# Kernel tuning notes

Hardware: AMD Instinct MI355X
Metric: run time of the kernel (lower is better)

## Reference

```python
import jax, jax.numpy as jnp
import numpy as np

EPS = 1e-5
K = 5


def _bn(h, g, b):
    # BatchNorm1d in training mode: batch stats over all dims except channels.
    ax = tuple(range(h.ndim - 1))
    mu = jnp.mean(h, axis=ax, keepdims=True)
    var = jnp.var(h, axis=ax, keepdims=True)
    return g * (h - mu) * jax.lax.rsqrt(var + EPS) + b


def _block(x, w, b, g, be):
    # Lin -> ReLU -> BN, as in MLP() helper
    return _bn(jax.nn.relu(x @ w + b), g, be)


def _knn_idx(x, k):
    # x: [B, P, D]; k nearest per point (includes self at distance 0)
    sq = jnp.sum(x * x, axis=-1)
    d2 = sq[:, :, None] + sq[:, None, :] - 2.0 * jnp.einsum('bpd,bqd->bpq', x, x)
    return jax.lax.top_k(-d2, k)[1]  # [B, P, k]


def _edge_conv(x, k, mlp_fn):
    # DynamicEdgeConv: recompute kNN graph on current features, gather
    # neighbor/center pairs, per-edge MLP on [x_i, x_j - x_i], max-aggregate.
    idx = _knn_idx(x, k)                                   # [B,P,k]
    xj = jax.vmap(lambda xb, ib: xb[ib])(x, idx)           # [B,P,k,D]
    xi = jnp.broadcast_to(x[:, :, None, :], xj.shape)
    e = jnp.concatenate([xi, xj - xi], axis=-1)            # [B,P,k,2D]
    return jnp.max(mlp_fn(e), axis=2)                      # max aggr -> [B,P,C]


def dec_forward(pos,
                c1w0, c1b0, c1g0, c1e0,
                c1w1, c1b1, c1g1, c1e1,
                c1w2, c1b2, c1g2, c1e2,
                c2w, c2b, c2g, c2e,
                l1w, l1b, l1g, l1e,
                m1w, m1b, m1g, m1e,
                m2w, m2b, m2g, m2e,
                m3w, m3b):
    mlp1 = lambda e: _block(_block(_block(e, c1w0, c1b0, c1g0, c1e0),
                                   c1w1, c1b1, c1g1, c1e1),
                            c1w2, c1b2, c1g2, c1e2)
    x1 = _edge_conv(pos, K, mlp1)                          # [B,P,64]
    x2 = _edge_conv(x1, K, lambda e: _block(e, c2w, c2b, c2g, c2e))  # [B,P,128]
    h = _block(jnp.concatenate([x1, x2], axis=-1), l1w, l1b, l1g, l1e)  # [B,P,1024]
    p = jnp.max(h, axis=1)                                 # global_max_pool -> [B,1024]
    p = _block(p, m1w, m1b, m1g, m1e)                      # dropout omitted (eval)
    p = _block(p, m2w, m2b, m2g, m2e)
    return p @ m3w + m3b                                   # [B, n_classes]


def setup_inputs() -> dict:
    key = jax.random.key(0)
    ks = jax.random.split(key, 12)
    B, P = 16, 2048

    def w(k, shape):
        return 0.05 * jax.random.normal(k, shape, jnp.float32)

    z = lambda c: jnp.zeros((c,), jnp.float32)
    o = lambda c: jnp.ones((c,), jnp.float32)

    d = {
        'pos': jax.random.normal(ks[0], (B, P, 3), jnp.float32),
        'c1w0': w(ks[1], (6, 64)), 'c1b0': z(64), 'c1g0': o(64), 'c1e0': z(64),
        'c1w1': w(ks[2], (64, 64)), 'c1b1': z(64), 'c1g1': o(64), 'c1e1': z(64),
        'c1w2': w(ks[3], (64, 64)), 'c1b2': z(64), 'c1g2': o(64), 'c1e2': z(64),
        'c2w': w(ks[4], (128, 128)), 'c2b': z(128), 'c2g': o(128), 'c2e': z(128),
        'l1w': w(ks[5], (192, 1024)), 'l1b': z(1024), 'l1g': o(1024), 'l1e': z(1024),
        'm1w': w(ks[6], (1024, 512)), 'm1b': z(512), 'm1g': o(512), 'm1e': z(512),
        'm2w': w(ks[7], (512, 256)), 'm2b': z(256), 'm2g': o(256), 'm2e': z(256),
        'm3w': w(ks[8], (256, 2)), 'm3b': z(2),
    }
    return d


def reference(pos,
              c1w0, c1b0, c1g0, c1e0,
              c1w1, c1b1, c1g1, c1e1,
              c1w2, c1b2, c1g2, c1e2,
              c2w, c2b, c2g, c2e,
              l1w, l1b, l1g, l1e,
              m1w, m1b, m1g, m1e,
              m2w, m2b, m2g, m2e,
              m3w, m3b):
    return dec_forward(pos,
                       c1w0, c1b0, c1g0, c1e0,
                       c1w1, c1b1, c1g1, c1e1,
                       c1w2, c1b2, c1g2, c1e2,
                       c2w, c2b, c2g, c2e,
                       l1w, l1b, l1g, l1e,
                       m1w, m1b, m1g, m1e,
                       m2w, m2b, m2g, m2e,
                       m3w, m3b)
```

## Files before the change

### kernel.cpp

```cpp
#include <hip/hip_runtime.h>
#include <cmath>

constexpr int B = 16, P = 2048, KNN = 5;
constexpr int BP = B * P;
constexpr int E = BP * KNN;
constexpr float EPS = 1e-5f;
constexpr int AS = 72;
constexpr int QC2 = 4;

constexpr int ST0 = 0;
constexpr int ST1 = 128;
constexpr int ST2 = 256;
constexpr int ST3 = 384;
constexpr int ST4 = 640;
constexpr int ST5 = 2688;
constexpr int ST6 = 3712;
constexpr int ST_TOTAL = 4224;

typedef __attribute__((ext_vector_type(8))) short bf16x8;
typedef __attribute__((ext_vector_type(4))) float f32x4;

__device__ inline unsigned short f2bf(float x) {
    unsigned u = __float_as_uint(x);
    unsigned r = (u + 0x7FFFu + ((u >> 16) & 1u)) >> 16;
    return (unsigned short)r;
}
__device__ inline void split2bf(float x, unsigned short& h, unsigned short& l) {
    unsigned short hh = f2bf(x);
    float fh = __uint_as_float(((unsigned)hh) << 16);
    h = hh;
    l = f2bf(x - fh);
}
__device__ inline void packsplit(float a, float b, unsigned& hi2, unsigned& lo2) {
    unsigned short ah, al, bh, bl;
    split2bf(a, ah, al); split2bf(b, bh, bl);
    hi2 = (unsigned)ah | ((unsigned)bh << 16);
    lo2 = (unsigned)al | ((unsigned)bl << 16);
}

__device__ inline void ins5(float d, int qi, float bd[KNN], int bi[KNN]) {
    bool c0 = d < bd[0], c1 = d < bd[1], c2 = d < bd[2], c3 = d < bd[3], c4 = d < bd[4];
    bd[4] = c3 ? bd[3] : (c4 ? d : bd[4]);  bi[4] = c3 ? bi[3] : (c4 ? qi : bi[4]);
    bd[3] = c2 ? bd[2] : (c3 ? d : bd[3]);  bi[3] = c2 ? bi[2] : (c3 ? qi : bi[3]);
    bd[2] = c1 ? bd[1] : (c2 ? d : bd[2]);  bi[2] = c1 ? bi[1] : (c2 ? qi : bi[2]);
    bd[1] = c0 ? bd[0] : (c1 ? d : bd[1]);  bi[1] = c0 ? bi[0] : (c1 ? qi : bi[1]);
    bd[0] = c0 ? d : bd[0];                 bi[0] = c0 ? qi : bi[0];
}
__device__ inline void ins5t(float d, int qi, float bd[KNN], int bi[KNN]) {
    bool c0 = (d < bd[0]) || (d == bd[0] && qi < bi[0]);
    bool c1 = (d < bd[1]) || (d == bd[1] && qi < bi[1]);
    bool c2 = (d < bd[2]) || (d == bd[2] && qi < bi[2]);
    bool c3 = (d < bd[3]) || (d == bd[3] && qi < bi[3]);
    bool c4 = (d < bd[4]) || (d == bd[4] && qi < bi[4]);
    bd[4] = c3 ? bd[3] : (c4 ? d : bd[4]);  bi[4] = c3 ? bi[3] : (c4 ? qi : bi[4]);
    bd[3] = c2 ? bd[2] : (c3 ? d : bd[3]);  bi[3] = c2 ? bi[2] : (c3 ? qi : bi[3]);
    bd[2] = c1 ? bd[1] : (c2 ? d : bd[2]);  bi[2] = c1 ? bi[1] : (c2 ? qi : bi[2]);
    bd[1] = c0 ? bd[0] : (c1 ? d : bd[1]);  bi[1] = c0 ? bi[0] : (c1 ? qi : bi[1]);
    bd[0] = c0 ? d : bd[0];                 bi[0] = c0 ? qi : bi[0];
}

__global__ void k_init(float* __restrict__ stats, float* __restrict__ pmax,
                       float* __restrict__ pmin) {
    int i = blockIdx.x * 256 + threadIdx.x;
    if (i < ST_TOTAL) stats[i] = 0.f;
    if (i < B * 1024) { pmax[i] = 0.f; pmin[i] = INFINITY; }
}

__global__ __launch_bounds__(256) void k_redstat(const float* __restrict__ part,
        float* __restrict__ stats, int nblk) {
    __shared__ float r[256];
    int slot = blockIdx.x;
    float s = 0.f;
    for (int i = threadIdx.x; i < nblk; i += 256)
        s += part[(size_t)i * 128 + slot];
    r[threadIdx.x] = s; __syncthreads();
    for (int o = 128; o; o >>= 1) {
        if (threadIdx.x < o) r[threadIdx.x] += r[threadIdx.x + o];
        __syncthreads();
    }
    if (threadIdx.x == 0) stats[slot] = r[0];
}

__global__ void k_wsplit(const float* __restrict__ w, unsigned short* __restrict__ th,
                         unsigned short* __restrict__ tl, int K, int N) {
    int i = blockIdx.x * 256 + threadIdx.x;
    if (i >= K * N) return;
    int k = i / N, n = i - k * N;
    float f = w[i];
    unsigned short h = f2bf(f);
    th[(size_t)n * K + k] = h;
    tl[(size_t)n * K + k] = f2bf(f - __uint_as_float((unsigned)h << 16));
}

__global__ void k_xsplit(const float* __restrict__ x, unsigned short* __restrict__ xh,
                         unsigned short* __restrict__ xl) {
    int i = blockIdx.x * 256 + threadIdx.x;
    float f = x[i];
    unsigned short h = f2bf(f);
    xh[i] = h;
    xl[i] = f2bf(f - __uint_as_float((unsigned)h << 16));
}

__global__ __launch_bounds__(256) void k_knn1(const float* __restrict__ pos,
                                              int* __restrict__ idx1) {
    __shared__ float4 qt[2048];
    int b = blockIdx.x >> 5;
    int p0 = (blockIdx.x & 31) << 6;
    const float* posb = pos + (size_t)b * P * 3;
#pragma unroll
    for (int t = 0; t < 8; ++t) {
        int q = (t << 8) + threadIdx.x;
        float qx = posb[q * 3 + 0], qy = posb[q * 3 + 1], qz = posb[q * 3 + 2];
        qt[q] = make_float4(qx, qy, qz, qx * qx + qy * qy + qz * qz);
    }
    __syncthreads();
    int pl = threadIdx.x >> 2, sub = threadIdx.x & 3;
    int p = p0 + pl;
    float4 me = qt[p];
    float x = me.x, y = me.y, z = me.z, sqp = me.w;
    float bd[KNN]; int bi[KNN];
#pragma unroll
    for (int i = 0; i < KNN; ++i) { bd[i] = INFINITY; bi[i] = 0; }
    for (int j0 = 0; j0 < 512; j0 += 8) {
        float4 v[8];
#pragma unroll
        for (int u = 0; u < 8; ++u) v[u] = qt[((j0 + u) << 2) | sub];
#pragma unroll
        for (int u = 0; u < 8; ++u) {
            float dot = x * v[u].x + y * v[u].y + z * v[u].z;
            float d2 = sqp + v[u].w - 2.f * dot;
            if (d2 < bd[KNN - 1]) ins5(d2, ((j0 + u) << 2) | sub, bd, bi);
        }
    }
#pragma unroll
    for (int w = 1; w <= 2; w <<= 1) {
        float od[KNN]; int oi[KNN];
#pragma unroll
        for (int i = 0; i < KNN; ++i) {
            od[i] = __shfl_xor(bd[i], w, 64);
            oi[i] = __shfl_xor(bi[i], w, 64);
        }
#pragma unroll
        for (int i = 0; i < KNN; ++i) ins5t(od[i], oi[i], bd, bi);
    }
    if (sub == 0) {
        size_t o = ((size_t)b * P + p) * KNN;
#pragma unroll
        for (int i = 0; i < KNN; ++i) idx1[o + i] = bi[i];
    }
}

__global__ __launch_bounds__(256) void k_ec1_l0(const float* __restrict__ pos,
        const int* __restrict__ idx1, const float* __restrict__ w,
        const float* __restrict__ bias, float* __restrict__ zout,
        float* __restrict__ part) {
    __shared__ float elds[256][6];
    __shared__ float red[256];
    int tid = threadIdx.x;
    int base = blockIdx.x * 256;
    {
        int e = base + tid;
        int bp = e / KNN;
        int bb = bp >> 11;
        int q = idx1[e];
        const float* pi = pos + (size_t)bp * 3;
        const float* pj = pos + ((size_t)(bb << 11) + q) * 3;
        float x0 = pi[0], x1v = pi[1], x2v = pi[2];
        elds[tid][0] = x0; elds[tid][1] = x1v; elds[tid][2] = x2v;
        elds[tid][3] = pj[0] - x0; elds[tid][4] = pj[1] - x1v; elds[tid][5] = pj[2] - x2v;
    }
    int c = tid & 63, lane = tid >> 6;
    float wr[6];
#pragma unroll
    for (int d = 0; d < 6; ++d) wr[d] = w[d * 64 + c];
    float bc = bias[c];
    __syncthreads();
    float s1 = 0.f, s2 = 0.f;
    for (int i = 0; i < 64; ++i) {
        int e = lane + (i << 2);
        float acc = bc;
#pragma unroll
        for (int d = 0; d < 6; ++d) acc = fmaf(elds[e][d], wr[d], acc);
        acc = fmaxf(acc, 0.f);
        zout[(size_t)(base + e) * 64 + c] = acc;
        s1 += acc; s2 = fmaf(acc, acc, s2);
    }
    red[tid] = s1; __syncthreads();
    if (tid < 64) part[(size_t)blockIdx.x * 128 + tid] =
        red[tid] + red[tid + 64] + red[tid + 128] + red[tid + 192];
    __syncthreads();
    red[tid] = s2; __syncthreads();
    if (tid < 64) part[(size_t)blockIdx.x * 128 + 64 + tid] =
        red[tid] + red[tid + 64] + red[tid + 128] + red[tid + 192];
}

__global__ __launch_bounds__(256) void k_lin64(const float* __restrict__ zin,
        const float* __restrict__ statsIn, const float* __restrict__ g,
        const float* __restrict__ be, const float* __restrict__ w,
        const float* __restrict__ bias, float* __restrict__ zout,
        float* __restrict__ part, float invN) {
    __shared__ __align__(16) float a[64 * 64];
    __shared__ float scl[64], shf[64];
    __shared__ float red[256];
    int tid = threadIdx.x;
    int base = blockIdx.x * 64;
    if (tid < 64) {
        float mu = statsIn[tid] * invN;
        float var = statsIn[64 + tid] * invN - mu * mu;
        float sc = g[tid] * rsqrtf(var + EPS);
        scl[tid] = sc; shf[tid] = be[tid] - mu * sc;
    }
    __syncthreads();
#pragma unroll
    for (int t = 0; t < 16; ++t) {
        int flat = tid + (t << 8);
        int k = flat & 63;
        a[flat] = fmaf(zin[(size_t)base * 64 + flat], scl[k], shf[k]);
    }
    int c = tid & 63, lane = tid >> 6;
    float wr[64];
#pragma unroll
    for (int k = 0; k < 64; ++k) wr[k] = w[k * 64 + c];
    float bc = bias[c];
    __syncthreads();
    float s1 = 0.f, s2 = 0.f;
    for (int i = 0; i < 16; ++i) {
        int e = lane + (i << 2);
        const float4* ap4 = (const float4*)(a + (e << 6));
        float acc = bc;
#pragma unroll
        for (int k4 = 0; k4 < 16; ++k4) {
            float4 v = ap4[k4];
            acc = fmaf(v.x, wr[k4 * 4 + 0], acc);
            acc = fmaf(v.y, wr[k4 * 4 + 1], acc);
            acc = fmaf(v.z, wr[k4 * 4 + 2], acc);
            acc = fmaf(v.w, wr[k4 * 4 + 3], acc);
        }
        acc = fmaxf(acc, 0.f);
        zout[(size_t)(base + e) * 64 + c] = acc;
        s1 += acc; s2 = fmaf(acc, acc, s2);
    }
    red[tid] = s1; __syncthreads();
    if (tid < 64) part[(size_t)blockIdx.x * 128 + tid] =
        red[tid] + red[tid + 64] + red[tid + 128] + red[tid + 192];
    __syncthreads();
    red[tid] = s2; __syncthreads();
    if (tid < 64) part[(size_t)blockIdx.x * 128 + 64 + tid] =
        red[tid] + red[tid + 64] + red[tid + 128] + red[tid + 192];
}

__global__ __launch_bounds__(256) void k_ec1_fin(const float* __restrict__ z2,
        const float* __restrict__ statsIn, const float* __restrict__ g,
        const float* __restrict__ be, float* __restrict__ x1,
        float* __restrict__ sq2) {
    int tid = threadIdx.x;
    int o = blockIdx.x * 256 + tid;
    int c = o & 63; int bp = o >> 6;
    float mu = statsIn[c] * (1.f / E);
    float var = statsIn[64 + c] * (1.f / E) - mu * mu;
    float sc = g[c] * rsqrtf(var + EPS);
    float sh = be[c] - mu * sc;
    float m = -INFINITY;
#pragma unroll
    for (int j = 0; j < KNN; ++j)
        m = fmaxf(m, fmaf(z2[((size_t)bp * KNN + j) * 64 + c], sc, sh));
    x1[o] = m;
    float ss = m * m;
#pragma unroll
    for (int off = 32; off; off >>= 1) ss += __shfl_down(ss, off, 64);
    if (c == 0) sq2[bp] = ss;
}

__global__ __launch_bounds__(128, 1) void k_knn2(const unsigned short* __restrict__ x1h,
        const unsigned short* __restrict__ x1l, const float* __restrict__ sq2,
        float* __restrict__ cd, int* __restrict__ ci) {
    __shared__ float S[2][32 * 129];
    int tid = threadIdx.x;
    int wv = tid >> 6, lane = tid & 63;
    int l15 = lane & 15, quad = lane >> 4;
    int qc = blockIdx.x & (QC2 - 1);
    int pt = blockIdx.x >> 2;
    int b = pt >> 5;
    int pw = ((pt & 31) << 6) + wv * 32;
    const size_t xbase = (size_t)b * P * 64;
    float* Sw = &S[wv][0];

    bf16x8 ah[2][2], al[2][2];
#pragma unroll
    for (int i = 0; i < 2; ++i)
#pragma unroll
        for (int kc = 0; kc < 2; ++kc) {
            size_t o = xbase + (size_t)(pw + i * 16 + l15) * 64 + kc * 32 + quad * 8;
            ah[i][kc] = *(const bf16x8*)&x1h[o];
            al[i][kc] = *(const bf16x8*)&x1l[o];
        }

    int half = lane >> 5;
    int pidx = lane & 31;
    float bd[KNN]; int bi[KNN];
#pragma unroll
    for (int i = 0; i < KNN; ++i) { bd[i] = INFINITY; bi[i] = 0; }

    int qlo = qc << 9;
    for (int t = 0; t < 4; ++t) {
        int q0 = qlo + (t << 7);
        float qsv[8];
#pragma unroll
        for (int j = 0; j < 8; ++j) qsv[j] = sq2[b * P + q0 + j * 16 + l15];
        f32x4 acc[2][8];
#pragma unroll
        for (int i = 0; i < 2; ++i)
#pragma unroll
            for (int j = 0; j < 8; ++j) acc[i][j] = (f32x4)0.f;
#pragma unroll
        for (int kc = 0; kc < 2; ++kc) {
            bf16x8 bh[8], bl[8];
#pragma unroll
            for (int j = 0; j < 8; ++j) {
                size_t o = xbase + (size_t)(q0 + j * 16 + l15) * 64 + kc * 32 + quad * 8;
                bh[j] = *(const bf16x8*)&x1h[o];
                bl[j] = *(const bf16x8*)&x1l[o];
            }
#pragma unroll
            for (int i = 0; i < 2; ++i)
#pragma unroll
                for (int j = 0; j < 8; ++j) {
                    acc[i][j] = __builtin_amdgcn_mfma_f32_16x16x32_bf16(ah[i][kc], bh[j], acc[i][j], 0, 0, 0);
                    acc[i][j] = __builtin_amdgcn_mfma_f32_16x16x32_bf16(ah[i][kc], bl[j], acc[i][j], 0, 0, 0);
                    acc[i][j] = __builtin_amdgcn_mfma_f32_16x16x32_bf16(al[i][kc], bh[j], acc[i][j], 0, 0, 0);
                }
        }
#pragma unroll
        for (int i = 0; i < 2; ++i)
#pragma unroll
            for (int j = 0; j < 8; ++j)
#pragma unroll
                for (int r = 0; r < 4; ++r) {
                    int pl = i * 16 + quad * 4 + r;
                    Sw[pl * 129 + j * 16 + l15] = fmaf(acc[i][j][r], -2.f, qsv[j]);
                }
        const float* row = Sw + pidx * 129 + half * 64;
        int qb = q0 + half * 64;
        for (int jj = 0; jj < 64; jj += 4) {
            float k0 = row[jj + 0], k1 = row[jj + 1], k2 = row[jj + 2], k3 = row[jj + 3];
            if (k0 < bd[4]) ins5(k0, qb + jj + 0, bd, bi);
            if (k1 < bd[4]) ins5(k1, qb + jj + 1, bd, bi);
            if (k2 < bd[4]) ins5(k2, qb + jj + 2, bd, bi);
            if (k3 < bd[4]) ins5(k3, qb + jj + 3, bd, bi);
        }
    }
#pragma unroll
    for (int i = 0; i < KNN; ++i) {
        float od = __shfl_xor(bd[i], 32, 64);
        int oi = __shfl_xor(bi[i], 32, 64);
        if (half == 0) ins5t(od, oi, bd, bi);
    }
    if (half == 0) {
        size_t o = (((size_t)b * P + pw + pidx) * QC2 + qc) * KNN;
#pragma unroll
        for (int i = 0; i < KNN; ++i) { cd[o + i] = bd[i]; ci[o + i] = bi[i]; }
    }
}

__global__ __launch_bounds__(256) void k_knn2m(const float* __restrict__ cd,
        const int* __restrict__ ci, int* __restrict__ idx2) {
    int bp = blockIdx.x * 256 + threadIdx.x;
    float bd[KNN]; int bi[KNN];
#pragma unroll
    for (int i = 0; i < KNN; ++i) { bd[i] = INFINITY; bi[i] = 0; }
    size_t o = (size_t)bp * QC2 * KNN;
    for (int t = 0; t < QC2 * KNN; ++t) {
        float d2 = cd[o + t]; int qi = ci[o + t];
        if (d2 < bd[KNN - 1]) ins5(d2, qi, bd, bi);
    }
#pragma unroll
    for (int i = 0; i < KNN; ++i) idx2[bp * KNN + i] = bi[i];
}

__global__ __launch_bounds__(256) void k_ec2m(const float* __restrict__ x1,
        const int* __restrict__ idx2,
        const unsigned short* __restrict__ wth, const unsigned short* __restrict__ wtl,
        const float* __restrict__ bias, float* __restrict__ zout,
        float* __restrict__ stats) {
    __shared__ unsigned short Ah[128 * AS], Al[128 * AS];
    __shared__ int rowI[128], rowJ[128];
    __shared__ float red[2 * 128 * 2];
    int tid = threadIdx.x;
    int base = blockIdx.x * 128;
    int bb = base / (P * KNN);
    if (tid < 128) {
        int e = base + tid;
        int bp = e / KNN;
        rowI[tid] = bp;
        rowJ[tid] = (bb << 11) + idx2[e];
    }
    int wv = tid >> 6, lane = tid & 63;
    int wm = wv >> 1, wn = wv & 1;
    int l15 = lane & 15, quad = lane >> 4;
    f32x4 acc[4][4];
#pragma unroll
    for (int i = 0; i < 4; ++i)
#pragma unroll
        for (int j = 0; j < 4; ++j) acc[i][j] = (f32x4)0.f;

    for (int k0 = 0; k0 < 128; k0 += 64) {
        __syncthreads();
#pragma unroll
        for (int i = 0; i < 16; ++i) {
            int pr = tid + (i << 8);
            int r = pr >> 5, kp = (pr & 31) << 1;
            float2 vi = *(const float2*)(x1 + (size_t)rowI[r] * 64 + kp);
            float2 v;
            if (k0 == 0) v = vi;
            else {
                float2 vj = *(const float2*)(x1 + (size_t)rowJ[r] * 64 + kp);
                v = make_float2(vj.x - vi.x, vj.y - vi.y);
            }
            unsigned h2, l2; packsplit(v.x, v.y, h2, l2);
            *(unsigned*)&Ah[r * AS + kp] = h2;
            *(unsigned*)&Al[r * AS + kp] = l2;
        }
        __syncthreads();
#pragma unroll
        for (int kc = 0; kc < 64; kc += 32) {
            bf16x8 afh[4], afl[4], bfh[4], bfl[4];
#pragma unroll
            for (int i = 0; i < 4; ++i) {
                int ro = (wm * 64 + i * 16 + l15) * AS + kc + quad * 8;
                afh[i] = *(const bf16x8*)&Ah[ro];
                afl[i] = *(const bf16x8*)&Al[ro];
            }
#pragma unroll
            for (int j = 0; j < 4; ++j) {
                size_t wo = (size_t)(wn * 64 + j * 16 + l15) * 128 + k0 + kc + quad * 8;
                bfh[j] = *(const bf16x8*)&wth[wo];
                bfl[j] = *(const bf16x8*)&wtl[wo];
            }
#pragma unroll
            for (int i = 0; i < 4; ++i)
#pragma unroll
                for (int j = 0; j < 4; ++j) {
                    acc[i][j] = __builtin_amdgcn_mfma_f32_16x16x32_bf16(afh[i], bfh[j], acc[i][j], 0, 0, 0);
                    acc[i][j] = __builtin_amdgcn_mfma_f32_16x16x32_bf16(afh[i], bfl[j], acc[i][j], 0, 0, 0);
                    acc[i][j] = __builtin_amdgcn_mfma_f32_16x16x32_bf16(afl[i], bfh[j], acc[i][j], 0, 0, 0);
                }
        }
    }
#pragma unroll
    for (int j = 0; j < 4; ++j) {
        int colL = wn * 64 + j * 16 + l15;
        float bl = bias[colL];
        float s1 = 0.f, s2 = 0.f;
#pragma unroll
        for (int i = 0; i < 4; ++i) {
            int row = wm * 64 + i * 16 + quad * 4;
#pragma unroll
            for (int r = 0; r < 4; ++r) {
                float v = fmaxf(acc[i][j][r] + bl, 0.f);
                zout[(size_t)(base + row + r) * 128 + colL] = v;
                s1 += v; s2 = fmaf(v, v, s2);
            }
        }
        s1 += __shfl_xor(s1, 16, 64); s1 += __shfl_xor(s1, 32, 64);
        s2 += __shfl_xor(s2, 16, 64); s2 += __shfl_xor(s2, 32, 64);
        if (quad == 0) {
            red[(wm * 128 + colL) * 2 + 0] = s1;
            red[(wm * 128 + colL) * 2 + 1] = s2;
        }
    }
    __syncthreads();
    if (tid < 128) {
        atomicAdd(&stats[tid], red[tid * 2] + red[(128 + tid) * 2]);
        atomicAdd(&stats[128 + tid], red[tid * 2 + 1] + red[(128 + tid) * 2 + 1]);
    }
}

__global__ __launch_bounds__(256) void k_ec2_fin(const float* __restrict__ z3,
        const float* __restrict__ stats, const float* __restrict__ g,
        const float* __restrict__ be, float* __restrict__ x2) {
    int o = blockIdx.x * 256 + threadIdx.x;
    int c = o & 127; int bp = o >> 7;
    float mu = stats[c] * (1.f / E);
    float var = stats[128 + c] * (1.f / E) - mu * mu;
    float sc = g[c] * rsqrtf(var + EPS);
    float sh = be[c] - mu * sc;
    float m = -INFINITY;
#pragma unroll
    for (int j = 0; j < KNN; ++j)
        m = fmaxf(m, fmaf(z3[((size_t)bp * KNN + j) * 128 + c], sc, sh));
    x2[o] = m;
}

__global__ __launch_bounds__(256) void k_l1m(
        const unsigned short* __restrict__ x1h, const unsigned short* __restrict__ x1l,
        const unsigned short* __restrict__ x2h, const unsigned short* __restrict__ x2l,
        const unsigned short* __restrict__ wth, const unsigned short* __restrict__ wtl,
        const float* __restrict__ bias, float* __restrict__ stats,
        float* __restrict__ pmax, float* __restrict__ pmin) {
    __shared__ float red[2 * 128 * 4];
    int tid = threadIdx.x;
    int brow = blockIdx.x & 255;
    int bcol = blockIdx.x >> 8;
    int row0 = brow << 7, col0 = bcol << 7;
    int wv = tid >> 6, lane = tid & 63;
    int wm = wv >> 1, wn = wv & 1;
    int l15 = lane & 15, quad = lane >> 4;
    f32x4 acc[4][4];
#pragma unroll
    for (int i = 0; i < 4; ++i)
#pragma unroll
        for (int j = 0; j < 4; ++j) acc[i][j] = (f32x4)0.f;

#pragma unroll
    for (int k0 = 0; k0 < 192; k0 += 32) {
        const unsigned short* ah = (k0 < 64) ? x1h : x2h;
        const unsigned short* al = (k0 < 64) ? x1l : x2l;
        int astr = (k0 < 64) ? 64 : 128;
        int aoff = (k0 < 64) ? k0 : (k0 - 64);
        bf16x8 afh[4], afl[4], bfh[4], bfl[4];
#pragma unroll
        for (int i = 0; i < 4; ++i) {
            size_t o = (size_t)(row0 + wm * 64 + i * 16 + l15) * astr + aoff + quad * 8;
            afh[i] = *(const bf16x8*)&ah[o];
            afl[i] = *(const bf16x8*)&al[o];
        }
#pragma unroll
        for (int j = 0; j < 4; ++j) {
            size_t wo = (size_t)(col0 + wn * 64 + j * 16 + l15) * 192 + k0 + quad * 8;
            bfh[j] = *(const bf16x8*)&wth[wo];
            bfl[j] = *(const bf16x8*)&wtl[wo];
        }
#pragma unroll
        for (int i = 0; i < 4; ++i)
#pragma unroll
            for (int j = 0; j < 4; ++j) {
                acc[i][j] = __builtin_amdgcn_mfma_f32_16x16x32_bf16(afh[i], bfh[j], acc[i][j], 0, 0, 0);
                acc[i][j] = __builtin_amdgcn_mfma_f32_16x16x32_bf16(afh[i], bfl[j], acc[i][j], 0, 0, 0);
                acc[i][j] = __builtin_amdgcn_mfma_f32_16x16x32_bf16(afl[i], bfh[j], acc[i][j], 0, 0, 0);
            }
    }
#pragma unroll
    for (int j = 0; j < 4; ++j) {
        int colL = wn * 64 + j * 16 + l15;
        float bl = bias[col0 + colL];
        float s1 = 0.f, s2 = 0.f, mx = 0.f, mn = INFINITY;
#pragma unroll
        for (int i = 0; i < 4; ++i)
#pragma unroll
            for (int r = 0; r < 4; ++r) {
                float v = fmaxf(acc[i][j][r] + bl, 0.f);
                s1 += v; s2 = fmaf(v, v, s2);
                mx = fmaxf(mx, v); mn = fminf(mn, v);
            }
        s1 += __shfl_xor(s1, 16, 64); s1 += __shfl_xor(s1, 32, 64);
        s2 += __shfl_xor(s2, 16, 64); s2 += __shfl_xor(s2, 32, 64);
        mx = fmaxf(mx, __shfl_xor(mx, 16, 64)); mx = fmaxf(mx, __shfl_xor(mx, 32, 64));
        mn = fminf(mn, __shfl_xor(mn, 16, 64)); mn = fminf(mn, __shfl_xor(mn, 32, 64));
        if (quad == 0) {
            float* rp = &red[(wm * 128 + colL) * 4];
            rp[0] = s1; rp[1] = s2; rp[2] = mx; rp[3] = mn;
        }
    }
    __syncthreads();
    if (tid < 128) {
        const float* r0 = &red[tid * 4];
        const float* r1 = &red[(128 + tid) * 4];
        int bb = row0 >> 11;
        atomicAdd(&stats[col0 + tid], r0[0] + r1[0]);
        atomicAdd(&stats[1024 + col0 + tid], r0[1] + r1[1]);
        atomicMax((unsigned int*)&pmax[bb * 1024 + col0 + tid],
                  __float_as_uint(fmaxf(r0[2], r1[2])));
        atomicMin((unsigned int*)&pmin[bb * 1024 + col0 + tid],
                  __float_as_uint(fminf(r0[3], r1[3])));
    }
}

__global__ void k_pool(const float* __restrict__ stats, const float* __restrict__ g,
                       const float* __restrict__ be, const float* __restrict__ pmax,
                       const float* __restrict__ pmin, float* __restrict__ p) {
    int o = blockIdx.x * 256 + threadIdx.x;
    int c = o & 1023;
    float mu = stats[c] * (1.f / BP);
    float var = stats[1024 + c] * (1.f / BP) - mu * mu;
    float sc = g[c] * rsqrtf(var + EPS);
    float sh = be[c] - mu * sc;
    float v = (sc >= 0.f) ? pmax[o] : pmin[o];
    p[o] = fmaf(v, sc, sh);
}

__global__ __launch_bounds__(256) void k_m1(const float* __restrict__ p,
        const float* __restrict__ w, const float* __restrict__ bias,
        float* __restrict__ t1, float* __restrict__ stats) {
    int o = blockIdx.x * 256 + threadIdx.x;
    int c = o & 511, b = o >> 9;
    const float* pr = p + (b << 10);
    float acc = bias[c];
    for (int k = 0; k < 1024; ++k) acc = fmaf(pr[k], w[k * 512 + c], acc);
    acc = fmaxf(acc, 0.f);
    t1[o] = acc;
    atomicAdd(&stats[c], acc);
    atomicAdd(&stats[512 + c], acc * acc);
}

__global__ __launch_bounds__(256) void k_m2(const float* __restrict__ t1,
        const float* __restrict__ stats5, const float* __restrict__ g,
        const float* __restrict__ be, const float* __restrict__ w,
        const float* __restrict__ bias, float* __restrict__ t2,
        float* __restrict__ stats6) {
    __shared__ float scl[512], shf[512];
    int tid = threadIdx.x;
    for (int t = tid; t < 512; t += 256) {
        float mu = stats5[t] * (1.f / 16.f);
        float var = stats5[512 + t] * (1.f / 16.f) - mu * mu;
        float sc = g[t] * rsqrtf(var + EPS);
        scl[t] = sc; shf[t] = be[t] - mu * sc;
    }
    __syncthreads();
    int o = blockIdx.x * 256 + tid;
    int c = o & 255, b = o >> 8;
    const float* tr = t1 + (b << 9);
    float acc = bias[c];
    for (int k = 0; k < 512; ++k) {
        float u = fmaf(tr[k], scl[k], shf[k]);
        acc = fmaf(u, w[k * 256 + c], acc);
    }
    acc = fmaxf(acc, 0.f);
    t2[o] = acc;
    atomicAdd(&stats6[c], acc);
    atomicAdd(&stats6[256 + c], acc * acc);
}

__global__ __launch_bounds__(256) void k_m3(const float* __restrict__ t2,
        const float* __restrict__ stats6, const float* __restrict__ g,
        const float* __restrict__ be, const float* __restrict__ w,
        const float* __restrict__ bias, float* __restrict__ out) {
    __shared__ float scl[256], shf[256];
    int tid = threadIdx.x;
    {
        float mu = stats6[tid] * (1.f / 16.f);
        float var = stats6[256 + tid] * (1.f / 16.f) - mu * mu;
        float sc = g[tid] * rsqrtf(var + EPS);
        scl[tid] = sc; shf[tid] = be[tid] - mu * sc;
    }
    __syncthreads();
    if (tid < 32) {
        int c = tid & 1, b = tid >> 1;
        const float* tr = t2 + (b << 8);
        float acc = bias[c];
        for (int k = 0; k < 256; ++k) {
            float u = fmaf(tr[k], scl[k], shf[k]);
            acc = fmaf(u, w[k * 2 + c], acc);
        }
        out[tid] = acc;
    }
}

extern "C" void kernel_launch(void* const* d_in, const int* in_sizes, int n_in,
                              void* d_out, int out_size, void* d_ws, size_t ws_size,
                              hipStream_t stream) {
    const float* pos  = (const float*)d_in[0];
    const float* c1w0 = (const float*)d_in[1];
    const float* c1b0 = (const float*)d_in[2];
    const float* c1g0 = (const float*)d_in[3];
    const float* c1e0 = (const float*)d_in[4];
    const float* c1w1 = (const float*)d_in[5];
    const float* c1b1 = (const float*)d_in[6];
    const float* c1g1 = (const float*)d_in[7];
    const float* c1e1 = (const float*)d_in[8];
    const float* c1w2 = (const float*)d_in[9];
    const float* c1b2 = (const float*)d_in[10];
    const float* c1g2 = (const float*)d_in[11];
    const float* c1e2 = (const float*)d_in[12];
    const float* c2w  = (const float*)d_in[13];
    const float* c2b  = (const float*)d_in[14];
    const float* c2g  = (const float*)d_in[15];
    const float* c2e  = (const float*)d_in[16];
    const float* l1w  = (const float*)d_in[17];
    const float* l1b  = (const float*)d_in[18];
    const float* l1g  = (const float*)d_in[19];
    const float* l1e  = (const float*)d_in[20];
    const float* m1w  = (const float*)d_in[21];
    const float* m1b  = (const float*)d_in[22];
    const float* m1g  = (const float*)d_in[23];
    const float* m1e  = (const float*)d_in[24];
    const float* m2w  = (const float*)d_in[25];
    const float* m2b  = (const float*)d_in[26];
    const float* m2g  = (const float*)d_in[27];
    const float* m2e  = (const float*)d_in[28];
    const float* m3w  = (const float*)d_in[29];
    const float* m3b  = (const float*)d_in[30];
    float* out = (float*)d_out;

    char* ws = (char*)d_ws;
    size_t off = 0;
    auto alloc = [&](size_t bytes) {
        size_t r = off; off = (off + bytes + 255) & ~(size_t)255; return r;
    };
    float* stats = (float*)(ws + alloc(ST_TOTAL * 4));
    float* pmax  = (float*)(ws + alloc(16 * 1024 * 4));
    float* pmin  = (float*)(ws + alloc(16 * 1024 * 4));
    float* pbuf  = (float*)(ws + alloc(16 * 1024 * 4));
    float* t1    = (float*)(ws + alloc(16 * 512 * 4));
    float* t2    = (float*)(ws + alloc(16 * 256 * 4));
    float* sq2   = (float*)(ws + alloc((size_t)BP * 4));
    float* part  = (float*)(ws + alloc((size_t)(E / 64) * 128 * 4));
    unsigned short* wthL = (unsigned short*)(ws + alloc((size_t)192 * 1024 * 2));
    unsigned short* wtlL = (unsigned short*)(ws + alloc((size_t)192 * 1024 * 2));
    unsigned short* wthC = (unsigned short*)(ws + alloc((size_t)128 * 128 * 2));
    unsigned short* wtlC = (unsigned short*)(ws + alloc((size_t)128 * 128 * 2));
    int*   idx1  = (int*)  (ws + alloc((size_t)E * 4));
    int*   idx2  = (int*)  (ws + alloc((size_t)E * 4));
    float* x1    = (float*)(ws + alloc((size_t)BP * 64 * 4));
    float* x2    = (float*)(ws + alloc((size_t)BP * 128 * 4));
    float* zA    = (float*)(ws + alloc((size_t)E * 128 * 4));
    float* zB    = (float*)(ws + alloc((size_t)E * 64 * 4));
    unsigned short* x1h = (unsigned short*)zB;
    unsigned short* x1l = x1h + (size_t)BP * 64;
    float* cand_d = (float*)(x1l + (size_t)BP * 64);
    int*   cand_i = (int*)(cand_d + (size_t)BP * QC2 * KNN);
    unsigned short* x2h = (unsigned short*)(cand_i + (size_t)BP * QC2 * KNN);
    unsigned short* x2l = x2h + (size_t)BP * 128;

    (void)in_sizes; (void)n_in; (void)out_size; (void)ws_size;

    k_init<<<64, 256, 0, stream>>>(stats, pmax, pmin);
    k_wsplit<<<(192 * 1024 + 255) / 256, 256, 0, stream>>>(l1w, wthL, wtlL, 192, 1024);
    k_wsplit<<<(128 * 128 + 255) / 256, 256, 0, stream>>>(c2w, wthC, wtlC, 128, 128);
    k_knn1<<<B * 32, 256, 0, stream>>>(pos, idx1);
    k_ec1_l0<<<E / 256, 256, 0, stream>>>(pos, idx1, c1w0, c1b0, zA, part);
    k_redstat<<<128, 256, 0, stream>>>(part, stats + ST0, E / 256);
    k_lin64<<<E / 64, 256, 0, stream>>>(zA, stats + ST0, c1g0, c1e0, c1w1, c1b1,
                                        zB, part, 1.f / E);
    k_redstat<<<128, 256, 0, stream>>>(part, stats + ST1, E / 64);
    k_lin64<<<E / 64, 256, 0, stream>>>(zB, stats + ST1, c1g1, c1e1, c1w2, c1b2,
                                        zA, part, 1.f / E);
    k_redstat<<<128, 256, 0, stream>>>(part, stats + ST2, E / 64);
    k_ec1_fin<<<BP * 64 / 256, 256, 0, stream>>>(zA, stats + ST2, c1g2, c1e2, x1, sq2);
    k_xsplit<<<BP * 64 / 256, 256, 0, stream>>>(x1, x1h, x1l);
    k_knn2<<<B * 32 * QC2, 128, 0, stream>>>(x1h, x1l, sq2, cand_d, cand_i);
    k_knn2m<<<BP / 256, 256, 0, stream>>>(cand_d, cand_i, idx2);
    k_ec2m<<<E / 128, 256, 0, stream>>>(x1, idx2, wthC, wtlC, c2b, zA, stats + ST3);
    k_ec2_fin<<<BP * 128 / 256, 256, 0, stream>>>(zA, stats + ST3, c2g, c2e, x2);
    k_xsplit<<<BP * 128 / 256, 256, 0, stream>>>(x2, x2h, x2l);
    k_l1m<<<256 * 8, 256, 0, stream>>>(x1h, x1l, x2h, x2l, wthL, wtlL, l1b,
                                       stats + ST4, pmax, pmin);
    k_pool<<<64, 256, 0, stream>>>(stats + ST4, l1g, l1e, pmax, pmin, pbuf);
    k_m1<<<32, 256, 0, stream>>>(pbuf, m1w, m1b, t1, stats + ST5);
    k_m2<<<16, 256, 0, stream>>>(t1, stats + ST5, m1g, m1e, m2w, m2b, t2, stats + ST6);
    k_m3<<<1, 256, 0, stream>>>(t2, stats + ST6, m2g, m2e, m3w, m3b, out);
}
```

Measured before the change: 678.2 us.

## Refactor edge-conv2 GEMM algebraically to use presplit x1 directly without LDS staging

Rewrites [x_i, x_j - x_i]·W as x_i·(W0-W1) + x_j·W1 by precomputing a split bf16 difference weight and second-half weight. The ec2 kernel then loads the already-split x1 hi/lo fragments straight from global memory into MFMA operands, removing the LDS staging, per-element bf16 splitting and block barriers. This trades the shared-memory path for gathered global loads issued by each wave and slightly changes rounding because the weight difference is formed before splitting.

```diff
diff --git a/kernel.cpp b/kernel.cpp
--- a/kernel.cpp
+++ b/kernel.cpp
@@ -5,7 +5,6 @@
 constexpr int BP = B * P;
 constexpr int E = BP * KNN;
 constexpr float EPS = 1e-5f;
-constexpr int AS = 72;
 constexpr int QC2 = 4;
 
 constexpr int ST0 = 0;
@@ -30,12 +29,6 @@
     float fh = __uint_as_float(((unsigned)hh) << 16);
     h = hh;
     l = f2bf(x - fh);
-}
-__device__ inline void packsplit(float a, float b, unsigned& hi2, unsigned& lo2) {
-    unsigned short ah, al, bh, bl;
-    split2bf(a, ah, al); split2bf(b, bh, bl);
-    hi2 = (unsigned)ah | ((unsigned)bh << 16);
-    lo2 = (unsigned)al | ((unsigned)bl << 16);
 }
 
 __device__ inline void ins5(float d, int qi, float bd[KNN], int bi[KNN]) {
@@ -90,6 +83,22 @@
     unsigned short h = f2bf(f);
     th[(size_t)n * K + k] = h;
     tl[(size_t)n * K + k] = f2bf(f - __uint_as_float((unsigned)h << 16));
+}
+
+__global__ void k_wprep2(const float* __restrict__ w,
+        unsigned short* __restrict__ wdh, unsigned short* __restrict__ wdl,
+        unsigned short* __restrict__ w1h, unsigned short* __restrict__ w1l) {
+    int i = blockIdx.x * 256 + threadIdx.x;
+    if (i >= 64 * 128) return;
+    int k = i >> 7, n = i & 127;
+    float w0 = w[k * 128 + n];
+    float w1 = w[(64 + k) * 128 + n];
+    float wd = w0 - w1;
+    unsigned short h;
+    h = f2bf(wd); wdh[n * 64 + k] = h;
+    wdl[n * 64 + k] = f2bf(wd - __uint_as_float((unsigned)h << 16));
+    h = f2bf(w1); w1h[n * 64 + k] = h;
+    w1l[n * 64 + k] = f2bf(w1 - __uint_as_float((unsigned)h << 16));
 }
 
 __global__ void k_xsplit(const float* __restrict__ x, unsigned short* __restrict__ xh,
@@ -377,64 +386,52 @@
     for (int i = 0; i < KNN; ++i) idx2[bp * KNN + i] = bi[i];
 }
 
-__global__ __launch_bounds__(256) void k_ec2m(const float* __restrict__ x1,
+__global__ __launch_bounds__(256) void k_ec2m(
+        const unsigned short* __restrict__ x1h, const unsigned short* __restrict__ x1l,
         const int* __restrict__ idx2,
-        const unsigned short* __restrict__ wth, const unsigned short* __restrict__ wtl,
+        const unsigned short* __restrict__ wdh, const unsigned short* __restrict__ wdl,
+        const unsigned short* __restrict__ w1h, const unsigned short* __restrict__ w1l,
         const float* __restrict__ bias, float* __restrict__ zout,
         float* __restrict__ stats) {
-    __shared__ unsigned short Ah[128 * AS], Al[128 * AS];
-    __shared__ int rowI[128], rowJ[128];
     __shared__ float red[2 * 128 * 2];
     int tid = threadIdx.x;
     int base = blockIdx.x * 128;
     int bb = base / (P * KNN);
-    if (tid < 128) {
-        int e = base + tid;
-        int bp = e / KNN;
-        rowI[tid] = bp;
-        rowJ[tid] = (bb << 11) + idx2[e];
-    }
     int wv = tid >> 6, lane = tid & 63;
     int wm = wv >> 1, wn = wv & 1;
     int l15 = lane & 15, quad = lane >> 4;
+    int rI[4], rJ[4];
+#pragma unroll
+    for (int i = 0; i < 4; ++i) {
+        int e = base + wm * 64 + i * 16 + l15;
+        rI[i] = e / KNN;
+        rJ[i] = (bb << 11) + idx2[e];
+    }
     f32x4 acc[4][4];
 #pragma unroll
     for (int i = 0; i < 4; ++i)
 #pragma unroll
         for (int j = 0; j < 4; ++j) acc[i][j] = (f32x4)0.f;
 
-    for (int k0 = 0; k0 < 128; k0 += 64) {
-        __syncthreads();
-#pragma unroll
-        for (int i = 0; i < 16; ++i) {
-            int pr = tid + (i << 8);
-            int r = pr >> 5, kp = (pr & 31) << 1;
-            float2 vi = *(const float2*)(x1 + (size_t)rowI[r] * 64 + kp);
-            float2 v;
-            if (k0 == 0) v = vi;
-            else {
-                float2 vj = *(const float2*)(x1 + (size_t)rowJ[r] * 64 + kp);
-                v = make_float2(vj.x - vi.x, vj.y - vi.y);
+#pragma unroll
+    for (int s = 0; s < 2; ++s) {
+        const unsigned short* bh_ = s ? w1h : wdh;
+        const unsigned short* bl_ = s ? w1l : wdl;
+#pragma unroll
+        for (int kc = 0; kc < 2; ++kc) {
+            bf16x8 afh[4], afl[4], bfh[4], bfl[4];
+#pragma unroll
+            for (int i = 0; i < 4; ++i) {
+                int row = s ? rJ[i] : rI[i];
+                size_t o = (size_t)row * 64 + kc * 32 + quad * 8;
+                afh[i] = *(const bf16x8*)&x1h[o];
+                afl[i] = *(const bf16x8*)&x1l[o];
             }
-            unsigned h2, l2; packsplit(v.x, v.y, h2, l2);
-            *(unsigned*)&Ah[r * AS + kp] = h2;
-            *(unsigned*)&Al[r * AS + kp] = l2;
-        }
-        __syncthreads();
-#pragma unroll
-        for (int kc = 0; kc < 64; kc += 32) {
-            bf16x8 afh[4], afl[4], bfh[4], bfl[4];
-#pragma unroll
-            for (int i = 0; i < 4; ++i) {
-                int ro = (wm * 64 + i * 16 + l15) * AS + kc + quad * 8;
-                afh[i] = *(const bf16x8*)&Ah[ro];
-                afl[i] = *(const bf16x8*)&Al[ro];
-            }
 #pragma unroll
             for (int j = 0; j < 4; ++j) {
-                size_t wo = (size_t)(wn * 64 + j * 16 + l15) * 128 + k0 + kc + quad * 8;
-                bfh[j] = *(const bf16x8*)&wth[wo];
-                bfl[j] = *(const bf16x8*)&wtl[wo];
+                size_t wo = (size_t)(wn * 64 + j * 16 + l15) * 64 + kc * 32 + quad * 8;
+                bfh[j] = *(const bf16x8*)&bh_[wo];
+                bfl[j] = *(const bf16x8*)&bl_[wo];
             }
 #pragma unroll
             for (int i = 0; i < 4; ++i)
@@ -706,8 +703,10 @@
     float* part  = (float*)(ws + alloc((size_t)(E / 64) * 128 * 4));
     unsigned short* wthL = (unsigned short*)(ws + alloc((size_t)192 * 1024 * 2));
     unsigned short* wtlL = (unsigned short*)(ws + alloc((size_t)192 * 1024 * 2));
-    unsigned short* wthC = (unsigned short*)(ws + alloc((size_t)128 * 128 * 2));
-    unsigned short* wtlC = (unsigned short*)(ws + alloc((size_t)128 * 128 * 2));
+    unsigned short* wdh  = (unsigned short*)(ws + alloc((size_t)128 * 64 * 2));
+    unsigned short* wdl  = (unsigned short*)(ws + alloc((size_t)128 * 64 * 2));
+    unsigned short* w1h  = (unsigned short*)(ws + alloc((size_t)128 * 64 * 2));
+    unsigned short* w1l  = (unsigned short*)(ws + alloc((size_t)128 * 64 * 2));
     int*   idx1  = (int*)  (ws + alloc((size_t)E * 4));
     int*   idx2  = (int*)  (ws + alloc((size_t)E * 4));
     float* x1    = (float*)(ws + alloc((size_t)BP * 64 * 4));
@@ -725,7 +724,7 @@
 
     k_init<<<64, 256, 0, stream>>>(stats, pmax, pmin);
     k_wsplit<<<(192 * 1024 + 255) / 256, 256, 0, stream>>>(l1w, wthL, wtlL, 192, 1024);
-    k_wsplit<<<(128 * 128 + 255) / 256, 256, 0, stream>>>(c2w, wthC, wtlC, 128, 128);
+    k_wprep2<<<(64 * 128 + 255) / 256, 256, 0, stream>>>(c2w, wdh, wdl, w1h, w1l);
     k_knn1<<<B * 32, 256, 0, stream>>>(pos, idx1);
     k_ec1_l0<<<E / 256, 256, 0, stream>>>(pos, idx1, c1w0, c1b0, zA, part);
     k_redstat<<<128, 256, 0, stream>>>(part, stats + ST0, E / 256);
@@ -739,7 +738,8 @@
     k_xsplit<<<BP * 64 / 256, 256, 0, stream>>>(x1, x1h, x1l);
     k_knn2<<<B * 32 * QC2, 128, 0, stream>>>(x1h, x1l, sq2, cand_d, cand_i);
     k_knn2m<<<BP / 256, 256, 0, stream>>>(cand_d, cand_i, idx2);
-    k_ec2m<<<E / 128, 256, 0, stream>>>(x1, idx2, wthC, wtlC, c2b, zA, stats + ST3);
+    k_ec2m<<<E / 128, 256, 0, stream>>>(x1h, x1l, idx2, wdh, wdl, w1h, w1l,
+                                        c2b, zA, stats + ST3);
     k_ec2_fin<<<BP * 128 / 256, 256, 0, stream>>>(zA, stats + ST3, c2g, c2e, x2);
     k_xsplit<<<BP * 128 / 256, 256, 0, stream>>>(x2, x2h, x2l);
     k_l1m<<<256 * 8, 256, 0, stream>>>(x1h, x1l, x2h, x2l, wthL, wtlL, l1b,
```

Measured after the change: 648.3 us. 4.4% less time.
